# Kernel optimization log

Measured on AMD Instinct MI355X. Metric: run time of the kernel, lower is better.

Reference implementation:

```python
import jax, jax.numpy as jnp
import numpy as np

N = 262144  # points per batch (~4096 rays x 64 samples)
FDIM = 64   # plane feature dim
S = 512     # base plane resolution


def setup_inputs() -> dict:
    key = jax.random.key(0)
    ks = jax.random.split(key, 10)
    x = jax.random.uniform(ks[0], (N, 3), dtype=jnp.float32, minval=-1.0, maxval=1.0)
    rays_o = jnp.array([[0.0, 0.0, 1.5]], dtype=jnp.float32)  # ray origin; distances straddle 1.5/2.0
    scale = jnp.ones((3,), dtype=jnp.float32)
    plane = lambda k, s: jax.random.normal(k, (FDIM, s, s), dtype=jnp.float32)
    return {
        'x': x, 'rays_o': rays_o, 'scale': scale,
        'xy_plane': plane(ks[1], S), 'yz_plane': plane(ks[2], S), 'xz_plane': plane(ks[3], S),
        'xy_plane1': plane(ks[4], S // 2), 'yz_plane1': plane(ks[5], S // 2), 'xz_plane1': plane(ks[6], S // 2),
        'xy_plane2': plane(ks[7], S // 4), 'yz_plane2': plane(ks[8], S // 4), 'xz_plane2': plane(ks[9], S // 4),
    }


def bilinear_sample(plane, coords):
    """F.grid_sample(mode='bilinear', align_corners=True, padding_mode='zeros').
    plane: [C, H, W]; coords: [N, 2] with (x, y) in [-1, 1] (x indexes W).
    Returns [N, C]."""
    C, H, W = plane.shape
    fx = (coords[:, 0] + 1.0) * 0.5 * (W - 1)
    fy = (coords[:, 1] + 1.0) * 0.5 * (H - 1)
    x0 = jnp.floor(fx)
    y0 = jnp.floor(fy)
    wx = fx - x0
    wy = fy - y0
    x0i = x0.astype(jnp.int32)
    y0i = y0.astype(jnp.int32)

    def gather(xi, yi):
        valid = (xi >= 0) & (xi < W) & (yi >= 0) & (yi < H)
        xc = jnp.clip(xi, 0, W - 1)
        yc = jnp.clip(yi, 0, H - 1)
        v = plane[:, yc, xc]  # [C, N]
        return jnp.where(valid[None, :], v, 0.0)

    v00 = gather(x0i, y0i)
    v01 = gather(x0i + 1, y0i)
    v10 = gather(x0i, y0i + 1)
    v11 = gather(x0i + 1, y0i + 1)
    out = (v00 * (1 - wx) * (1 - wy) + v01 * wx * (1 - wy)
           + v10 * (1 - wx) * wy + v11 * wx * wy)  # [C, N]
    return out.T


def forward(x, rays_o, scale, xy0, yz0, xz0, xy1, yz1, xz1, xy2, yz2, xz2):
    xs = x * scale[None, :]
    xy_c = xs[:, :2]                                   # (x, y)
    xz_c = jnp.stack([xs[:, 0], xs[:, 2]], axis=-1)    # (x, z)
    yz_c = xs[:, 1:]                                   # (y, z)

    # laplace breakpoints: first index with distance > 1.5 / > 2.0 from rays_o[0]
    d = jnp.linalg.norm(rays_o[0][None, :] - xs, axis=-1)
    c1 = d > 1.5
    c2 = d > 2.0
    break1 = jnp.where(c1.any(), jnp.argmax(c1), 0)
    break2 = jnp.where(c2.any(), jnp.argmax(c2), 0)
    idx = jnp.arange(x.shape[0])
    # level 0: [0, break1), level 1: [break1, break2), level 2: [break2, N)
    level = jnp.where(idx < break1, 0, jnp.where(idx < break2, 1, 2))[:, None]

    def tri(p0, p1, p2, c):
        s0 = bilinear_sample(p0, c)
        s1 = bilinear_sample(p1, c)
        s2 = bilinear_sample(p2, c)
        # laplace: level1 = fine + half, level2 = fine + half + quarter
        return jnp.where(level == 0, s0, jnp.where(level == 1, s0 + s1, s0 + s1 + s2))

    return (tri(xy0, xy1, xy2, xy_c)
            + tri(xz0, xz1, xz2, xz_c)
            + tri(yz0, yz1, yz2, yz_c))


def reference(x, rays_o, scale, xy_plane, yz_plane, xz_plane, xy_plane1, yz_plane1, xz_plane1, xy_plane2, yz_plane2, xz_plane2):
    return forward(x, rays_o, scale, xy_plane, yz_plane, xz_plane,
                   xy_plane1, yz_plane1, xz_plane1,
                   xy_plane2, yz_plane2, xz_plane2)
```

## Files before the change

kernel.cpp:

```cpp
#include <hip/hip_runtime.h>
#include <hip/hip_fp16.h>

#define NPTS 262144
#define FDIM 64
#define NCELL 4096

typedef float vfloat4 __attribute__((ext_vector_type(4)));

__global__ __launch_bounds__(256) void break_kernel(const float* __restrict__ x,
                                                    const float* __restrict__ rays_o,
                                                    const float* __restrict__ scale,
                                                    unsigned* __restrict__ breaks) {
  const unsigned t = blockIdx.x * 256u + threadIdx.x;
  const float r0 = rays_o[0], r1 = rays_o[1], r2 = rays_o[2];
  const float s0 = scale[0], s1 = scale[1], s2 = scale[2];
  unsigned b1 = 0xFFFFFFFFu, b2 = 0xFFFFFFFFu;
  for (unsigned p = t; p < NPTS; p += 65536u) {
    const float dx = r0 - x[p * 3 + 0] * s0;
    const float dy = r1 - x[p * 3 + 1] * s1;
    const float dz = r2 - x[p * 3 + 2] * s2;
    const float d = sqrtf(__fadd_rn(__fadd_rn(__fmul_rn(dx, dx), __fmul_rn(dy, dy)),
                                    __fmul_rn(dz, dz)));
    if (d > 1.5f) b1 = min(b1, p);
    if (d > 2.0f) b2 = min(b2, p);
  }
#pragma unroll
  for (int o = 32; o > 0; o >>= 1) {
    b1 = min(b1, (unsigned)__shfl_down((int)b1, o, 64));
    b2 = min(b2, (unsigned)__shfl_down((int)b2, o, 64));
  }
  if ((threadIdx.x & 63) == 0) {
    atomicMin(&breaks[0], b1);
    atomicMin(&breaks[1], b2);
  }
}

__device__ __forceinline__ unsigned part4(unsigned v) {
  v &= 15u;
  v = (v | (v << 4)) & 0x0C3u;
  v = (v | (v << 2)) & 0x249u;
  return v;
}

__device__ __forceinline__ unsigned cell_key(float x0, float x1, float x2) {
  const int cx = min(max((int)((x0 + 1.0f) * 8.0f), 0), 15);
  const int cy = min(max((int)((x1 + 1.0f) * 8.0f), 0), 15);
  const int cz = min(max((int)((x2 + 1.0f) * 8.0f), 0), 15);
  return part4((unsigned)cx) | (part4((unsigned)cy) << 1) | (part4((unsigned)cz) << 2);
}

__global__ __launch_bounds__(256) void breakhist_kernel(const float* __restrict__ x,
                                                        const float* __restrict__ rays_o,
                                                        const float* __restrict__ scale,
                                                        unsigned* __restrict__ breaks,
                                                        unsigned* __restrict__ hist) {
  const unsigned t = blockIdx.x * 256u + threadIdx.x;
  const float s0 = scale[0], s1 = scale[1], s2 = scale[2];
  const float xs0 = x[t * 3 + 0] * s0;
  const float xs1 = x[t * 3 + 1] * s1;
  const float xs2 = x[t * 3 + 2] * s2;
  const float dx = rays_o[0] - xs0;
  const float dy = rays_o[1] - xs1;
  const float dz = rays_o[2] - xs2;
  const float d = sqrtf(__fadd_rn(__fadd_rn(__fmul_rn(dx, dx), __fmul_rn(dy, dy)),
                                  __fmul_rn(dz, dz)));
  unsigned b1 = (d > 1.5f) ? t : 0xFFFFFFFFu;
  unsigned b2 = (d > 2.0f) ? t : 0xFFFFFFFFu;
#pragma unroll
  for (int o = 32; o > 0; o >>= 1) {
    b1 = min(b1, (unsigned)__shfl_down((int)b1, o, 64));
    b2 = min(b2, (unsigned)__shfl_down((int)b2, o, 64));
  }
  if ((threadIdx.x & 63) == 0) {
    atomicMin(&breaks[0], b1);
    atomicMin(&breaks[1], b2);
  }
  const unsigned key = cell_key(xs0, xs1, xs2);
  atomicAdd(&hist[key], 1u);
}

__global__ __launch_bounds__(1024) void scan_kernel(unsigned* __restrict__ hist) {
  const int tid = threadIdx.x;
  uint4 h = ((uint4*)hist)[tid];
  const unsigned i0 = h.x;
  const unsigned i1 = i0 + h.y;
  const unsigned i2 = i1 + h.z;
  const unsigned i3 = i2 + h.w;
  __shared__ unsigned ls[1024];
  ls[tid] = i3;
  __syncthreads();
  for (int d = 1; d < 1024; d <<= 1) {
    const unsigned add = (tid >= d) ? ls[tid - d] : 0u;
    __syncthreads();
    ls[tid] += add;
    __syncthreads();
  }
  const unsigned base = ls[tid] - i3;
  uint4 o;
  o.x = base;
  o.y = base + i0;
  o.z = base + i1;
  o.w = base + i2;
  ((uint4*)hist)[tid] = o;
}

__global__ __launch_bounds__(256) void scatter_kernel(const float* __restrict__ x,
                                                      const float* __restrict__ scale,
                                                      const unsigned* __restrict__ breaks,
                                                      unsigned* __restrict__ offs,
                                                      float4* __restrict__ xs_sorted) {
  const unsigned t = blockIdx.x * 256u + threadIdx.x;
  const float s0 = scale[0], s1 = scale[1], s2 = scale[2];
  const float xs0 = x[t * 3 + 0] * s0;
  const float xs1 = x[t * 3 + 1] * s1;
  const float xs2 = x[t * 3 + 2] * s2;
  const unsigned key = cell_key(xs0, xs1, xs2);
  const unsigned pos = atomicAdd(&offs[key], 1u);
  unsigned b1 = breaks[0]; if (b1 >= NPTS) b1 = 0;
  unsigned b2 = breaks[1]; if (b2 >= NPTS) b2 = 0;
  const unsigned lvl = (t < b1) ? 0u : ((t < b2) ? 1u : 2u);
  float4 v;
  v.x = xs0; v.y = xs1; v.z = xs2;
  v.w = __uint_as_float(t | (lvl << 18));
  xs_sorted[pos] = v;
}

#define TPIX 128

struct TransposeArgs {
  const float* src[9];
  __half* dst[9];
  int tile_hi[9];
  int SS[9];
};

union H8 { uint4 u; __half h[8]; };

__global__ __launch_bounds__(256) void transpose_all(TransposeArgs a) {
  const int tile = blockIdx.x;
  int pi = 0;
#pragma unroll
  for (int i = 0; i < 9; ++i) {
    if (tile >= a.tile_hi[i]) pi = i + 1;
  }
  const int lo = (pi == 0) ? 0 : a.tile_hi[pi - 1];
  const float* __restrict__ src = a.src[pi];
  __half* __restrict__ dst = a.dst[pi];
  const size_t SS = (size_t)a.SS[pi];

  const int ntm = (int)(SS / TPIX) - 1;
  const int tl = ((tile - lo) * 997) & ntm;

  const int t = threadIdx.x;
  const int slot = t >> 3;
  const int c8 = t & 7;
  const size_t p0 = (size_t)tl * TPIX + (size_t)slot * 4;
  const float* __restrict__ srcb = src + (size_t)(c8 * 8) * SS + p0;

  H8 h[4];
#pragma unroll
  for (int k = 0; k < 8; ++k) {
    const float4 v = *(const float4*)(srcb + (size_t)k * SS);
    h[0].h[k] = __float2half(v.x);
    h[1].h[k] = __float2half(v.y);
    h[2].h[k] = __float2half(v.z);
    h[3].h[k] = __float2half(v.w);
  }
#pragma unroll
  for (int r = 0; r < 4; ++r) {
    *(uint4*)(dst + (p0 + (size_t)r) * FDIM + c8 * 8) = h[r].u;
  }
}

__device__ __forceinline__ void bilinear_weights(int W, float cx, float cy,
                                                 float& w00, float& w01, float& w10, float& w11,
                                                 int& xc0, int& xc1, int& yc0, int& yc1) {
  const float Wm1 = (float)(W - 1);
  const float fx = (cx + 1.0f) * 0.5f * Wm1;
  const float fy = (cy + 1.0f) * 0.5f * Wm1;
  const float x0f = floorf(fx), y0f = floorf(fy);
  const float wx = fx - x0f, wy = fy - y0f;
  const int ix = (int)x0f, iy = (int)y0f;
  const int ix1 = ix + 1, iy1 = iy + 1;
  const bool vx0 = (ix >= 0) && (ix < W);
  const bool vx1 = (ix1 >= 0) && (ix1 < W);
  const bool vy0 = (iy >= 0) && (iy < W);
  const bool vy1 = (iy1 >= 0) && (iy1 < W);
  xc0 = min(max(ix, 0), W - 1);
  xc1 = min(max(ix1, 0), W - 1);
  yc0 = min(max(iy, 0), W - 1);
  yc1 = min(max(iy1, 0), W - 1);
  w00 = (1.0f - wx) * (1.0f - wy) * (float)(vx0 && vy0);
  w01 = wx * (1.0f - wy) * (float)(vx1 && vy0);
  w10 = (1.0f - wx) * wy * (float)(vx0 && vy1);
  w11 = wx * wy * (float)(vx1 && vy1);
}

__device__ __forceinline__ void sample8_t(const __half* __restrict__ pl, int W,
                                          float cx, float cy, int j8, float acc[8]) {
  float w00, w01, w10, w11;
  int xc0, xc1, yc0, yc1;
  bilinear_weights(W, cx, cy, w00, w01, w10, w11, xc0, xc1, yc0, yc1);
  const __half* b00 = pl + ((size_t)(yc0 * W + xc0) * FDIM + j8);
  const __half* b01 = pl + ((size_t)(yc0 * W + xc1) * FDIM + j8);
  const __half* b10 = pl + ((size_t)(yc1 * W + xc0) * FDIM + j8);
  const __half* b11 = pl + ((size_t)(yc1 * W + xc1) * FDIM + j8);
  H8 v00, v01, v10, v11;
  v00.u = *(const uint4*)b00;
  v01.u = *(const uint4*)b01;
  v10.u = *(const uint4*)b10;
  v11.u = *(const uint4*)b11;
#pragma unroll
  for (int k = 0; k < 8; ++k) {
    acc[k] += w00 * __half2float(v00.h[k]) + w01 * __half2float(v01.h[k]) +
              w10 * __half2float(v10.h[k]) + w11 * __half2float(v11.h[k]);
  }
}

__device__ __forceinline__ void sample8_d(const float* __restrict__ pl, int W,
                                          float cx, float cy, int j8, float acc[8]) {
  float w00, w01, w10, w11;
  int xc0, xc1, yc0, yc1;
  bilinear_weights(W, cx, cy, w00, w01, w10, w11, xc0, xc1, yc0, yc1);
  const size_t SS = (size_t)W * W;
  const int i00 = yc0 * W + xc0, i01 = yc0 * W + xc1;
  const int i10 = yc1 * W + xc0, i11 = yc1 * W + xc1;
#pragma unroll
  for (int k = 0; k < 8; ++k) {
    const size_t co = (size_t)(j8 + k) * SS;
    acc[k] += w00 * pl[co + i00] + w01 * pl[co + i01] +
              w10 * pl[co + i10] + w11 * pl[co + i11];
  }
}

struct PlanesH { const __half* p[9]; };
struct PlanesF { const float* p[9]; };

#define SAMPLE_BLOCKS (NPTS * 8 / 256)
#define XCD_CHUNK (SAMPLE_BLOCKS / 8)

__global__ __launch_bounds__(256) void sample_kernel(const float4* __restrict__ xs_sorted,
                                                     PlanesH tp, float* __restrict__ out) {
  const unsigned b = blockIdx.x;
  const unsigned sb = (b & 7u) * XCD_CHUNK + (b >> 3);
  const int t = (int)(sb * 256u + threadIdx.x);
  const int slot = t >> 3;
  const int j8 = (t & 7) * 8;
  const float4 ps = xs_sorted[slot];
  const unsigned w = __float_as_uint(ps.w);
  const int p = (int)(w & 0x3FFFFu);
  const int level = (int)(w >> 18);
  float acc[8];
#pragma unroll
  for (int k = 0; k < 8; ++k) acc[k] = 0.0f;
  sample8_t(tp.p[0], 512, ps.x, ps.y, j8, acc);
  sample8_t(tp.p[1], 512, ps.y, ps.z, j8, acc);
  sample8_t(tp.p[2], 512, ps.x, ps.z, j8, acc);
  if (level >= 1) {
    sample8_t(tp.p[3], 256, ps.x, ps.y, j8, acc);
    sample8_t(tp.p[4], 256, ps.y, ps.z, j8, acc);
    sample8_t(tp.p[5], 256, ps.x, ps.z, j8, acc);
  }
  if (level >= 2) {
    sample8_t(tp.p[6], 128, ps.x, ps.y, j8, acc);
    sample8_t(tp.p[7], 128, ps.y, ps.z, j8, acc);
    sample8_t(tp.p[8], 128, ps.x, ps.z, j8, acc);
  }
  float* o = out + (size_t)p * FDIM + j8;
  vfloat4 lo = {acc[0], acc[1], acc[2], acc[3]};
  vfloat4 hi = {acc[4], acc[5], acc[6], acc[7]};
  __builtin_nontemporal_store(lo, (vfloat4*)o);
  __builtin_nontemporal_store(hi, (vfloat4*)(o + 4));
}

__global__ __launch_bounds__(256) void sample_kernel_direct(const float* __restrict__ x,
                                                            const float* __restrict__ scale,
                                                            const unsigned* __restrict__ breaks,
                                                            PlanesF tp, float* __restrict__ out) {
  const int t = blockIdx.x * 256 + threadIdx.x;
  const int p = t >> 3;
  const int j8 = (t & 7) * 8;
  const float s0 = scale[0], s1 = scale[1], s2 = scale[2];
  const float xs0 = x[p * 3 + 0] * s0;
  const float xs1 = x[p * 3 + 1] * s1;
  const float xs2 = x[p * 3 + 2] * s2;
  unsigned b1 = breaks[0]; if (b1 >= NPTS) b1 = 0;
  unsigned b2 = breaks[1]; if (b2 >= NPTS) b2 = 0;
  const unsigned pu = (unsigned)p;
  const int level = (pu < b1) ? 0 : ((pu < b2) ? 1 : 2);
  float acc[8];
#pragma unroll
  for (int k = 0; k < 8; ++k) acc[k] = 0.0f;
  sample8_d(tp.p[0], 512, xs0, xs1, j8, acc);
  sample8_d(tp.p[1], 512, xs1, xs2, j8, acc);
  sample8_d(tp.p[2], 512, xs0, xs2, j8, acc);
  if (level >= 1) {
    sample8_d(tp.p[3], 256, xs0, xs1, j8, acc);
    sample8_d(tp.p[4], 256, xs1, xs2, j8, acc);
    sample8_d(tp.p[5], 256, xs0, xs2, j8, acc);
  }
  if (level >= 2) {
    sample8_d(tp.p[6], 128, xs0, xs1, j8, acc);
    sample8_d(tp.p[7], 128, xs1, xs2, j8, acc);
    sample8_d(tp.p[8], 128, xs0, xs2, j8, acc);
  }
  float4* o4 = (float4*)(out + (size_t)p * FDIM + j8);
  o4[0] = make_float4(acc[0], acc[1], acc[2], acc[3]);
  o4[1] = make_float4(acc[4], acc[5], acc[6], acc[7]);
}

extern "C" void kernel_launch(void* const* d_in, const int* in_sizes, int n_in,
                              void* d_out, int out_size, void* d_ws, size_t ws_size,
                              hipStream_t stream) {
  const float* x = (const float*)d_in[0];
  const float* rays_o = (const float*)d_in[1];
  const float* scale = (const float*)d_in[2];
  const float* pl32[9];
  for (int i = 0; i < 9; ++i) pl32[i] = (const float*)d_in[3 + i];
  float* out = (float*)d_out;

  unsigned char* ws = (unsigned char*)d_ws;
  unsigned* breaks = (unsigned*)ws;
  unsigned* hist = (unsigned*)(ws + 1024);
  float4* xs_sorted = (float4*)(ws + 1024 + NCELL * 4);
  const size_t planes_off = 1024 + (size_t)NCELL * 4 + (size_t)NPTS * 16;

  (void)hipMemsetAsync(d_ws, 0xFF, 8, stream);

  const int Ss[3] = {512, 256, 128};
  size_t need = planes_off;
  for (int l = 0; l < 3; ++l) need += 3 * (size_t)Ss[l] * Ss[l] * FDIM * sizeof(__half);

  if (ws_size >= need) {
    (void)hipMemsetAsync(hist, 0, NCELL * 4, stream);
    breakhist_kernel<<<NPTS / 256, 256, 0, stream>>>(x, rays_o, scale, breaks, hist);
    scan_kernel<<<1, 1024, 0, stream>>>(hist);
    scatter_kernel<<<NPTS / 256, 256, 0, stream>>>(x, scale, breaks, hist, xs_sorted);

    PlanesH tp;
    TransposeArgs ta;
    size_t off = planes_off;
    int tiles_acc = 0;
    for (int l = 0; l < 3; ++l) {
      const int S = Ss[l];
      const int SS = S * S;
      for (int o = 0; o < 3; ++o) {
        const int i = l * 3 + o;
        __half* dst = (__half*)(ws + off);
        tp.p[i] = dst;
        ta.src[i] = pl32[i];
        ta.dst[i] = dst;
        ta.SS[i] = SS;
        tiles_acc += SS / TPIX;
        ta.tile_hi[i] = tiles_acc;
        off += (size_t)SS * FDIM * sizeof(__half);
      }
    }
    transpose_all<<<tiles_acc, 256, 0, stream>>>(ta);
    sample_kernel<<<SAMPLE_BLOCKS, 256, 0, stream>>>(xs_sorted, tp, out);
  } else {
    break_kernel<<<256, 256, 0, stream>>>(x, rays_o, scale, breaks);
    PlanesF tf;
    for (int i = 0; i < 9; ++i) tf.p[i] = pl32[i];
    sample_kernel_direct<<<(NPTS * 8) / 256, 256, 0, stream>>>(x, scale, breaks, tf, out);
  }
}
```

Baseline: 486.7 us.

## Fuse break/histogram with plane transpose and sort indices instead of coordinates

Merges the break-detection/histogram kernel and the plane transpose into a single launch with block-range dispatch. The break search now uses atomicMax on NPTS-t, so one zero memset covers both the breaks and the histogram. The scatter now writes only a packed 4-byte index plus level instead of a float4, and the sample kernel re-reads x through that index. This cuts launches, memsets and scatter traffic, at the cost of an indirect gather of x in the sampler.

```diff
diff --git a/kernel.cpp b/kernel.cpp
--- a/kernel.cpp
+++ b/kernel.cpp
@@ -49,34 +49,84 @@
   return part4((unsigned)cx) | (part4((unsigned)cy) << 1) | (part4((unsigned)cz) << 2);
 }
 
-__global__ __launch_bounds__(256) void breakhist_kernel(const float* __restrict__ x,
-                                                        const float* __restrict__ rays_o,
-                                                        const float* __restrict__ scale,
-                                                        unsigned* __restrict__ breaks,
-                                                        unsigned* __restrict__ hist) {
-  const unsigned t = blockIdx.x * 256u + threadIdx.x;
-  const float s0 = scale[0], s1 = scale[1], s2 = scale[2];
-  const float xs0 = x[t * 3 + 0] * s0;
-  const float xs1 = x[t * 3 + 1] * s1;
-  const float xs2 = x[t * 3 + 2] * s2;
-  const float dx = rays_o[0] - xs0;
-  const float dy = rays_o[1] - xs1;
-  const float dz = rays_o[2] - xs2;
-  const float d = sqrtf(__fadd_rn(__fadd_rn(__fmul_rn(dx, dx), __fmul_rn(dy, dy)),
-                                  __fmul_rn(dz, dz)));
-  unsigned b1 = (d > 1.5f) ? t : 0xFFFFFFFFu;
-  unsigned b2 = (d > 2.0f) ? t : 0xFFFFFFFFu;
-#pragma unroll
-  for (int o = 32; o > 0; o >>= 1) {
-    b1 = min(b1, (unsigned)__shfl_down((int)b1, o, 64));
-    b2 = min(b2, (unsigned)__shfl_down((int)b2, o, 64));
-  }
-  if ((threadIdx.x & 63) == 0) {
-    atomicMin(&breaks[0], b1);
-    atomicMin(&breaks[1], b2);
-  }
-  const unsigned key = cell_key(xs0, xs1, xs2);
-  atomicAdd(&hist[key], 1u);
+#define NB_BH (NPTS / 256)
+#define TPIX 128
+
+struct TransposeArgs {
+  const float* src[9];
+  __half* dst[9];
+  int tile_hi[9];
+  int SS[9];
+};
+
+union H8 { uint4 u; __half h[8]; };
+
+__global__ __launch_bounds__(256) void fused_bh_transpose(const float* __restrict__ x,
+                                                          const float* __restrict__ rays_o,
+                                                          const float* __restrict__ scale,
+                                                          unsigned* __restrict__ breaks,
+                                                          unsigned* __restrict__ hist,
+                                                          TransposeArgs a) {
+  const int bid = blockIdx.x;
+  if (bid < NB_BH) {
+    const unsigned t = (unsigned)bid * 256u + threadIdx.x;
+    const float s0 = scale[0], s1 = scale[1], s2 = scale[2];
+    const float xs0 = x[t * 3 + 0] * s0;
+    const float xs1 = x[t * 3 + 1] * s1;
+    const float xs2 = x[t * 3 + 2] * s2;
+    const float dx = rays_o[0] - xs0;
+    const float dy = rays_o[1] - xs1;
+    const float dz = rays_o[2] - xs2;
+    const float d = sqrtf(__fadd_rn(__fadd_rn(__fmul_rn(dx, dx), __fmul_rn(dy, dy)),
+                                    __fmul_rn(dz, dz)));
+    unsigned m1 = (d > 1.5f) ? (NPTS - t) : 0u;
+    unsigned m2 = (d > 2.0f) ? (NPTS - t) : 0u;
+#pragma unroll
+    for (int o = 32; o > 0; o >>= 1) {
+      m1 = max(m1, (unsigned)__shfl_down((int)m1, o, 64));
+      m2 = max(m2, (unsigned)__shfl_down((int)m2, o, 64));
+    }
+    if ((threadIdx.x & 63) == 0) {
+      atomicMax(&breaks[0], m1);
+      atomicMax(&breaks[1], m2);
+    }
+    const unsigned key = cell_key(xs0, xs1, xs2);
+    atomicAdd(&hist[key], 1u);
+    return;
+  }
+  const int tile = bid - NB_BH;
+  int pi = 0;
+#pragma unroll
+  for (int i = 0; i < 9; ++i) {
+    if (tile >= a.tile_hi[i]) pi = i + 1;
+  }
+  const int lo = (pi == 0) ? 0 : a.tile_hi[pi - 1];
+  const float* __restrict__ src = a.src[pi];
+  __half* __restrict__ dst = a.dst[pi];
+  const size_t SS = (size_t)a.SS[pi];
+
+  const int ntm = (int)(SS / TPIX) - 1;
+  const int tl = ((tile - lo) * 997) & ntm;
+
+  const int t = threadIdx.x;
+  const int slot = t >> 3;
+  const int c8 = t & 7;
+  const size_t p0 = (size_t)tl * TPIX + (size_t)slot * 4;
+  const float* __restrict__ srcb = src + (size_t)(c8 * 8) * SS + p0;
+
+  H8 h[4];
+#pragma unroll
+  for (int k = 0; k < 8; ++k) {
+    const float4 v = *(const float4*)(srcb + (size_t)k * SS);
+    h[0].h[k] = __float2half(v.x);
+    h[1].h[k] = __float2half(v.y);
+    h[2].h[k] = __float2half(v.z);
+    h[3].h[k] = __float2half(v.w);
+  }
+#pragma unroll
+  for (int r = 0; r < 4; ++r) {
+    *(uint4*)(dst + (p0 + (size_t)r) * FDIM + c8 * 8) = h[r].u;
+  }
 }
 
 __global__ __launch_bounds__(1024) void scan_kernel(unsigned* __restrict__ hist) {
@@ -108,7 +158,7 @@
                                                       const float* __restrict__ scale,
                                                       const unsigned* __restrict__ breaks,
                                                       unsigned* __restrict__ offs,
-                                                      float4* __restrict__ xs_sorted) {
+                                                      unsigned* __restrict__ order) {
   const unsigned t = blockIdx.x * 256u + threadIdx.x;
   const float s0 = scale[0], s1 = scale[1], s2 = scale[2];
   const float xs0 = x[t * 3 + 0] * s0;
@@ -116,60 +166,10 @@
   const float xs2 = x[t * 3 + 2] * s2;
   const unsigned key = cell_key(xs0, xs1, xs2);
   const unsigned pos = atomicAdd(&offs[key], 1u);
-  unsigned b1 = breaks[0]; if (b1 >= NPTS) b1 = 0;
-  unsigned b2 = breaks[1]; if (b2 >= NPTS) b2 = 0;
+  unsigned b1 = NPTS - breaks[0]; if (b1 >= NPTS) b1 = 0;
+  unsigned b2 = NPTS - breaks[1]; if (b2 >= NPTS) b2 = 0;
   const unsigned lvl = (t < b1) ? 0u : ((t < b2) ? 1u : 2u);
-  float4 v;
-  v.x = xs0; v.y = xs1; v.z = xs2;
-  v.w = __uint_as_float(t | (lvl << 18));
-  xs_sorted[pos] = v;
-}
-
-#define TPIX 128
-
-struct TransposeArgs {
-  const float* src[9];
-  __half* dst[9];
-  int tile_hi[9];
-  int SS[9];
-};
-
-union H8 { uint4 u; __half h[8]; };
-
-__global__ __launch_bounds__(256) void transpose_all(TransposeArgs a) {
-  const int tile = blockIdx.x;
-  int pi = 0;
-#pragma unroll
-  for (int i = 0; i < 9; ++i) {
-    if (tile >= a.tile_hi[i]) pi = i + 1;
-  }
-  const int lo = (pi == 0) ? 0 : a.tile_hi[pi - 1];
-  const float* __restrict__ src = a.src[pi];
-  __half* __restrict__ dst = a.dst[pi];
-  const size_t SS = (size_t)a.SS[pi];
-
-  const int ntm = (int)(SS / TPIX) - 1;
-  const int tl = ((tile - lo) * 997) & ntm;
-
-  const int t = threadIdx.x;
-  const int slot = t >> 3;
-  const int c8 = t & 7;
-  const size_t p0 = (size_t)tl * TPIX + (size_t)slot * 4;
-  const float* __restrict__ srcb = src + (size_t)(c8 * 8) * SS + p0;
-
-  H8 h[4];
-#pragma unroll
-  for (int k = 0; k < 8; ++k) {
-    const float4 v = *(const float4*)(srcb + (size_t)k * SS);
-    h[0].h[k] = __float2half(v.x);
-    h[1].h[k] = __float2half(v.y);
-    h[2].h[k] = __float2half(v.z);
-    h[3].h[k] = __float2half(v.w);
-  }
-#pragma unroll
-  for (int r = 0; r < 4; ++r) {
-    *(uint4*)(dst + (p0 + (size_t)r) * FDIM + c8 * 8) = h[r].u;
-  }
+  order[pos] = t | (lvl << 18);
 }
 
 __device__ __forceinline__ void bilinear_weights(int W, float cx, float cy,
@@ -239,32 +239,37 @@
 #define SAMPLE_BLOCKS (NPTS * 8 / 256)
 #define XCD_CHUNK (SAMPLE_BLOCKS / 8)
 
-__global__ __launch_bounds__(256) void sample_kernel(const float4* __restrict__ xs_sorted,
+__global__ __launch_bounds__(256) void sample_kernel(const float* __restrict__ x,
+                                                     const float* __restrict__ scale,
+                                                     const unsigned* __restrict__ order,
                                                      PlanesH tp, float* __restrict__ out) {
   const unsigned b = blockIdx.x;
   const unsigned sb = (b & 7u) * XCD_CHUNK + (b >> 3);
   const int t = (int)(sb * 256u + threadIdx.x);
   const int slot = t >> 3;
   const int j8 = (t & 7) * 8;
-  const float4 ps = xs_sorted[slot];
-  const unsigned w = __float_as_uint(ps.w);
-  const int p = (int)(w & 0x3FFFFu);
-  const int level = (int)(w >> 18);
+  const unsigned pk = order[slot];
+  const int p = (int)(pk & 0x3FFFFu);
+  const int level = (int)(pk >> 18);
+  const float s0 = scale[0], s1 = scale[1], s2 = scale[2];
+  const float xs0 = x[p * 3 + 0] * s0;
+  const float xs1 = x[p * 3 + 1] * s1;
+  const float xs2 = x[p * 3 + 2] * s2;
   float acc[8];
 #pragma unroll
   for (int k = 0; k < 8; ++k) acc[k] = 0.0f;
-  sample8_t(tp.p[0], 512, ps.x, ps.y, j8, acc);
-  sample8_t(tp.p[1], 512, ps.y, ps.z, j8, acc);
-  sample8_t(tp.p[2], 512, ps.x, ps.z, j8, acc);
+  sample8_t(tp.p[0], 512, xs0, xs1, j8, acc);
+  sample8_t(tp.p[1], 512, xs1, xs2, j8, acc);
+  sample8_t(tp.p[2], 512, xs0, xs2, j8, acc);
   if (level >= 1) {
-    sample8_t(tp.p[3], 256, ps.x, ps.y, j8, acc);
-    sample8_t(tp.p[4], 256, ps.y, ps.z, j8, acc);
-    sample8_t(tp.p[5], 256, ps.x, ps.z, j8, acc);
+    sample8_t(tp.p[3], 256, xs0, xs1, j8, acc);
+    sample8_t(tp.p[4], 256, xs1, xs2, j8, acc);
+    sample8_t(tp.p[5], 256, xs0, xs2, j8, acc);
   }
   if (level >= 2) {
-    sample8_t(tp.p[6], 128, ps.x, ps.y, j8, acc);
-    sample8_t(tp.p[7], 128, ps.y, ps.z, j8, acc);
-    sample8_t(tp.p[8], 128, ps.x, ps.z, j8, acc);
+    sample8_t(tp.p[6], 128, xs0, xs1, j8, acc);
+    sample8_t(tp.p[7], 128, xs1, xs2, j8, acc);
+    sample8_t(tp.p[8], 128, xs0, xs2, j8, acc);
   }
   float* o = out + (size_t)p * FDIM + j8;
   vfloat4 lo = {acc[0], acc[1], acc[2], acc[3]};
@@ -321,21 +326,16 @@
 
   unsigned char* ws = (unsigned char*)d_ws;
   unsigned* breaks = (unsigned*)ws;
-  unsigned* hist = (unsigned*)(ws + 1024);
-  float4* xs_sorted = (float4*)(ws + 1024 + NCELL * 4);
-  const size_t planes_off = 1024 + (size_t)NCELL * 4 + (size_t)NPTS * 16;
-
-  (void)hipMemsetAsync(d_ws, 0xFF, 8, stream);
+  unsigned* hist = (unsigned*)(ws + 256);
+  unsigned* order = (unsigned*)(ws + 256 + NCELL * 4);
+  const size_t planes_off = 256 + (size_t)NCELL * 4 + (size_t)NPTS * 4;
 
   const int Ss[3] = {512, 256, 128};
   size_t need = planes_off;
   for (int l = 0; l < 3; ++l) need += 3 * (size_t)Ss[l] * Ss[l] * FDIM * sizeof(__half);
 
   if (ws_size >= need) {
-    (void)hipMemsetAsync(hist, 0, NCELL * 4, stream);
-    breakhist_kernel<<<NPTS / 256, 256, 0, stream>>>(x, rays_o, scale, breaks, hist);
-    scan_kernel<<<1, 1024, 0, stream>>>(hist);
-    scatter_kernel<<<NPTS / 256, 256, 0, stream>>>(x, scale, breaks, hist, xs_sorted);
+    (void)hipMemsetAsync(d_ws, 0, 256 + NCELL * 4, stream);
 
     PlanesH tp;
     TransposeArgs ta;
@@ -356,9 +356,13 @@
         off += (size_t)SS * FDIM * sizeof(__half);
       }
     }
-    transpose_all<<<tiles_acc, 256, 0, stream>>>(ta);
-    sample_kernel<<<SAMPLE_BLOCKS, 256, 0, stream>>>(xs_sorted, tp, out);
+    fused_bh_transpose<<<NB_BH + tiles_acc, 256, 0, stream>>>(x, rays_o, scale,
+                                                              breaks, hist, ta);
+    scan_kernel<<<1, 1024, 0, stream>>>(hist);
+    scatter_kernel<<<NPTS / 256, 256, 0, stream>>>(x, scale, breaks, hist, order);
+    sample_kernel<<<SAMPLE_BLOCKS, 256, 0, stream>>>(x, scale, order, tp, out);
   } else {
+    (void)hipMemsetAsync(d_ws, 0xFF, 8, stream);
     break_kernel<<<256, 256, 0, stream>>>(x, rays_o, scale, breaks);
     PlanesF tf;
     for (int i = 0; i < 9; ++i) tf.p[i] = pl32[i];
```

Measured after the change: 474.9 us. 1.02x faster.
